# Performance work log

Measured on AMD Instinct MI355X. Metric: run time of the kernel, lower is better.

## Reference

```python
import math
import jax, jax.numpy as jnp
import numpy as np

B, M, N = 32, 64, 5000   # batch, multi_width (POMO rollouts), n_nodes
L, H, D, E = 100, 8, 16, 128  # local_size, head_num, qkv_dim, emb_dim


def setup_inputs() -> dict:
    key = jax.random.key(0)
    ks = jax.random.split(key, 10)
    return {
        "dist": jax.random.uniform(ks[0], (B, M, N), jnp.float32),
        "theta": jax.random.uniform(ks[1], (B, M, N), jnp.float32, minval=-math.pi, maxval=math.pi),
        "ninf_mask": jnp.zeros((B, M, N), jnp.float32),
        "W_init": jax.random.normal(ks[2], (E, 2), jnp.float32) * 0.1,
        "b_init": jax.random.normal(ks[3], (E,), jnp.float32) * 0.1,
        "cur_token": jax.random.uniform(ks[4], (E,), jnp.float32, minval=-1.0, maxval=1.0),
        "Wq": jax.random.normal(ks[5], (H * D, E), jnp.float32) * 0.05,
        "Wk": jax.random.normal(ks[6], (H * D, E), jnp.float32) * 0.05,
        "Wv": jax.random.normal(ks[7], (H * D, E), jnp.float32) * 0.05,
        "Wc": jax.random.normal(ks[8], (E, H * D), jnp.float32) * 0.05,
        "bc": jax.random.normal(ks[9], (E,), jnp.float32) * 0.05,
    }


def _positional_signal():
    # transformer sinusoidal encoding over the L gathered neighbors (E even -> no pad)
    num_ts = E // 2
    log_inc = math.log(10000.0) / max(num_ts - 1, 1)
    inv_ts = jnp.exp(jnp.arange(num_ts, dtype=jnp.float32) * -log_inc)
    pos = jnp.arange(L, dtype=jnp.float32)
    scaled = pos[:, None] * inv_ts[None, :]            # [L, E/2]
    return jnp.concatenate([jnp.sin(scaled), jnp.cos(scaled)], axis=1)  # [L, E]


def reference(dist, theta, ninf_mask, W_init, b_init, cur_token, Wq, Wk, Wv, Wc, bc):
    # mask out infeasible nodes (dist - (-inf) = +inf pushes them out of top-k)
    d = dist - ninf_mask                               # [B, M, N]
    neg_vals, idx = jax.lax.top_k(-d, L)               # smallest-L distances
    sorted_dist = -neg_vals                            # [B, M, L] ascending
    sorted_mask = jnp.take_along_axis(ninf_mask, idx, axis=-1)
    norm = sorted_dist.max(axis=-1, keepdims=True) + 1e-6
    sorted_dist = sorted_dist / norm
    sorted_theta = jnp.take_along_axis(theta, idx, axis=-1)
    sdt = jnp.stack([sorted_dist, sorted_theta], axis=-1)   # [B, M, L, 2]

    init_k = sdt @ W_init.T + b_init + _positional_signal()  # [B, M, L, E]

    # current-token query is a single shared learned vector -> q is [H, D]
    q = (Wq @ cur_token).reshape(H, D)
    kh = (init_k @ Wk.T).reshape(B, M, L, H, D)
    vh = (init_k @ Wv.T).reshape(B, M, L, H, D)

    score = jnp.einsum('hd,bmlhd->bhml', q, kh) / jnp.sqrt(jnp.float32(D))
    score = score + sorted_mask[:, None, :, :]              # rank3 ninf mask
    w = jax.nn.softmax(score, axis=-1)                      # [B, H, M, L]
    att = jnp.einsum('bhml,bmlhd->bmhd', w, vh).reshape(B, M, H * D)
    mh = att @ Wc.T + bc                                    # [B, M, E]

    score2 = jnp.einsum('bme,bmle->bml', mh, init_k) / jnp.sqrt(jnp.float32(E))

    # scatter local scores back into full [B, M, N]
    bi = jnp.arange(B)[:, None, None]
    mi = jnp.arange(M)[None, :, None]
    out = jnp.zeros((B, M, N), jnp.float32).at[bi, mi, idx].set(score2)
    return out
```

## Files before the change

### kernel.cpp

```cpp
#include <hip/hip_runtime.h>
#include <math.h>

#define B_ 32
#define M_ 64
#define N_ 5000
#define L_ 100
#define H_ 8
#define D_ 16
#define E_ 128
#define NBIN 2048
#define NT 512
#define NI4 1250

#define OFF_POSQ  0
#define OFF_C0    800
#define OFF_C1    808
#define OFF_C2    816
#define OFF_PV0   824
#define OFF_PV1   952
#define OFF_PVB   1080
#define OFF_WC0   1208
#define OFF_WC1   1336
#define OFF_WCB   1464
#define OFF_SB    1592
#define OFF_PCB   1596
#define OFF_PV    1696
#define OFF_PCT   14496

__device__ __forceinline__ int vbin(float v) {
  if (!(v >= 0.f)) return 0;
  if (v >= 1.0f) return NBIN - 1;
  return (int)(v * (float)NBIN);
}
__device__ __forceinline__ unsigned int umap(float v) {
  unsigned int b = __float_as_uint(v);
  return (b & 0x80000000u) ? ~b : (b | 0x80000000u);
}

__global__ __launch_bounds__(128) void precomp(
    const float* __restrict__ Wq, const float* __restrict__ Wk,
    const float* __restrict__ cur, const float* __restrict__ Wi,
    const float* __restrict__ bi, const float* __restrict__ Wv,
    const float* __restrict__ Wc, const float* __restrict__ bc,
    float* __restrict__ ws)
{
  const int tid = threadIdx.x;
  const int blk = blockIdx.x;
  __shared__ float pr[E_];
  __shared__ float red[8];
  const int lane = tid & 63, wv = tid >> 6;

  if (blk == 0) {
    float qsv = 0.f;
    for (int e = 0; e < E_; ++e) qsv = fmaf(Wq[tid * E_ + e], cur[e], qsv);
    float wk0=0,wk1=0,wkb=0,pv0=0,pv1=0,pvb=0,wc0=0,wc1=0,wcb=0;
    for (int e = 0; e < E_; ++e) {
      float wi0 = Wi[2*e], wi1 = Wi[2*e+1], bie = bi[e];
      float wk = Wk[tid*E_+e], wvv = Wv[tid*E_+e], wcc = Wc[e*(H_*D_)+tid];
      wk0=fmaf(wk,wi0,wk0);  wk1=fmaf(wk,wi1,wk1);  wkb=fmaf(wk,bie,wkb);
      pv0=fmaf(wvv,wi0,pv0); pv1=fmaf(wvv,wi1,pv1); pvb=fmaf(wvv,bie,pvb);
      wc0=fmaf(wcc,wi0,wc0); wc1=fmaf(wcc,wi1,wc1); wcb=fmaf(wcc,bie,wcb);
    }
    ws[OFF_PV0+tid]=pv0; ws[OFF_PV1+tid]=pv1; ws[OFF_PVB+tid]=pvb;
    ws[OFF_WC0+tid]=wc0; ws[OFF_WC1+tid]=wc1; ws[OFF_WCB+tid]=wcb;
    float c0 = qsv*wk0, c1 = qsv*wk1, c2 = qsv*wkb;
    for (int off = 1; off < 16; off <<= 1) {
      c0 += __shfl_xor(c0, off, 16); c1 += __shfl_xor(c1, off, 16); c2 += __shfl_xor(c2, off, 16);
    }
    if ((tid & 15) == 0) {
      int h = tid >> 4;
      ws[OFF_C0+h] = c0*0.25f; ws[OFF_C1+h] = c1*0.25f; ws[OFF_C2+h] = c2*0.25f;
    }
    float p0 = Wi[2*tid]*bc[tid], p1 = Wi[2*tid+1]*bc[tid], p2 = bi[tid]*bc[tid];
    for (int off = 32; off > 0; off >>= 1) {
      p0 += __shfl_xor(p0, off, 64); p1 += __shfl_xor(p1, off, 64); p2 += __shfl_xor(p2, off, 64);
    }
    if (lane == 0) { red[wv*3+0]=p0; red[wv*3+1]=p1; red[wv*3+2]=p2; }
    __syncthreads();
    if (tid == 0) {
      ws[OFF_SB+0]=red[0]+red[3]; ws[OFF_SB+1]=red[1]+red[4]; ws[OFF_SB+2]=red[2]+red[5];
    }
  } else {
    const int l = blk - 1;
    const float log_inc = 0.14619588050755848f;
    {
      int j = tid & 63;
      float scaled = (float)l * expf(-(float)j * log_inc);
      pr[tid] = (tid < 64) ? sinf(scaled) : cosf(scaled);
    }
    __syncthreads();
    float qsv=0.f, pwk=0.f, accv=0.f, accc=0.f;
    for (int e = 0; e < E_; ++e) qsv = fmaf(Wq[tid*E_+e], cur[e], qsv);
    for (int e = 0; e < E_; ++e) {
      float p = pr[e];
      pwk  = fmaf(Wk[tid*E_+e], p, pwk);
      accv = fmaf(Wv[tid*E_+e], p, accv);
      accc = fmaf(Wc[e*(H_*D_)+tid], p, accc);
    }
    ws[OFF_PV  + l*(H_*D_) + tid] = accv;
    ws[OFF_PCT + tid*L_ + l] = accc;
    float pq = qsv * pwk;
    for (int off = 1; off < 16; off <<= 1) pq += __shfl_xor(pq, off, 16);
    if ((tid & 15) == 0) ws[OFF_POSQ + (tid>>4)*L_ + l] = pq * 0.25f;
    float pb = pr[tid] * bc[tid];
    for (int off = 32; off > 0; off >>= 1) pb += __shfl_xor(pb, off, 64);
    if (lane == 0) red[wv] = pb;
    __syncthreads();
    if (tid == 0) ws[OFF_PCB + l] = red[0] + red[1];
  }
}

union alignas(16) SU {
  struct { unsigned short bins[N_]; unsigned int hist[NBIN]; } s;
  float rowbuf[N_];
  struct { float score[H_ * L_]; } a;
};

__global__ __launch_bounds__(NT, 8) void local_att_kernel(
    const float* __restrict__ dist, const float* __restrict__ theta,
    const float* __restrict__ ninf, const float* __restrict__ ws,
    float* __restrict__ out)
{
  __shared__ SU su;
  __shared__ unsigned long long sel64[128];
  __shared__ float sdv[128];
  __shared__ int idxs[128];
  __shared__ float stv[L_], smv[L_];
  __shared__ float att[H_ * D_], a0s[H_], a1s[H_];
  __shared__ unsigned int wsum[8];
  __shared__ int s_bstar;
  __shared__ unsigned int s_cumB, s_binc, s_chosen, s_cumb2, s_cnt;
  __shared__ float s_m0, s_m1, s_mb;

  const int tid = threadIdx.x;
  const int lane = tid & 63, wv = tid >> 6;
  const size_t base = (size_t)blockIdx.x * N_;
  const float4* d4 = (const float4*)(dist + base);
  const float4* n4 = (const float4*)(ninf + base);

  for (int j = tid; j < NBIN; j += NT) su.s.hist[j] = 0u;
  if (tid < 128) sel64[tid] = ~0ull;
  if (tid == 0) s_cnt = 0u;
  __syncthreads();

#pragma unroll
  for (int k = 0; k < 3; ++k) {
    int i4 = tid + k * NT;
    if (i4 < NI4) {
      float4 dv = d4[i4], nv = n4[i4];
      float vv4[4] = {dv.x - nv.x, dv.y - nv.y, dv.z - nv.z, dv.w - nv.w};
      unsigned int bn[4];
#pragma unroll
      for (int c = 0; c < 4; ++c) {
        bn[c] = (unsigned int)vbin(vv4[c]);
        atomicAdd(&su.s.hist[bn[c]], 1u);
      }
      uint2 pk;
      pk.x = bn[0] | (bn[1] << 16);
      pk.y = bn[2] | (bn[3] << 16);
      *(uint2*)&su.s.bins[i4 * 4] = pk;
    }
  }
  __syncthreads();

  unsigned int h4[4]; unsigned int s = 0u;
#pragma unroll
  for (int k2 = 0; k2 < 4; ++k2) { h4[k2] = su.s.hist[tid * 4 + k2]; s += h4[k2]; }
  unsigned int v = s;
  for (int off = 1; off < 64; off <<= 1) { unsigned int x = __shfl_up(v, off, 64); if (lane >= off) v += x; }
  if (lane == 63) wsum[wv] = v;
  __syncthreads();
  { unsigned int add = 0; for (int ww = 0; ww < wv; ++ww) add += wsum[ww]; v += add; }
  {
    unsigned int cumB = v - s;
    if (cumB < (unsigned)L_ && v >= (unsigned)L_) {
      unsigned int c = cumB;
#pragma unroll
      for (int k2 = 0; k2 < 4; ++k2) {
        unsigned int hh = h4[k2];
        if (c + hh >= (unsigned)L_) { s_bstar = tid * 4 + k2; s_cumB = c; s_binc = hh; break; }
        c += hh;
      }
    }
  }
  __syncthreads();
  const int bstar = s_bstar;
  const bool fb = (s_cumB + s_binc > 128u);
  unsigned long long kpiv = ~0ull;

  if (fb) {
    unsigned long long prefix = 0ull; unsigned int Krem = L_;
    for (int pass = 0; pass < 6; ++pass) {
      const int shift = 40 - 8 * pass;
      for (int j2 = tid; j2 < 256; j2 += NT) su.s.hist[j2] = 0u;
      __syncthreads();
#pragma unroll
      for (int k = 0; k < 3; ++k) {
        int i4 = tid + k * NT;
        if (i4 < NI4) {
          float4 dv = d4[i4], nv = n4[i4];
          float vv4[4] = {dv.x - nv.x, dv.y - nv.y, dv.z - nv.z, dv.w - nv.w};
#pragma unroll
          for (int c = 0; c < 4; ++c) {
            unsigned long long key = ((unsigned long long)umap(vv4[c]) << 16) | (unsigned)(i4 * 4 + c);
            if ((key >> (shift + 8)) == prefix)
              atomicAdd(&su.s.hist[(unsigned)(key >> shift) & 0xFFu], 1u);
          }
        }
      }
      __syncthreads();
      unsigned int ss = (tid < 256) ? su.s.hist[tid] : 0u;
      unsigned int vv = ss;
      for (int off = 1; off < 64; off <<= 1) { unsigned int x = __shfl_up(vv, off, 64); if (lane >= off) vv += x; }
      if (lane == 63) wsum[wv] = vv;
      __syncthreads();
      { unsigned int ad = 0; for (int ww = 0; ww < wv; ++ww) ad += wsum[ww]; vv += ad; }
      unsigned int cb = vv - ss;
      if (tid < 256 && cb < Krem && vv >= Krem) { s_chosen = (unsigned)tid; s_cumb2 = cb; }
      __syncthreads();
      prefix = (prefix << 8) | s_chosen;
      Krem -= s_cumb2;
      __syncthreads();
    }
    kpiv = prefix;
  }

#pragma unroll
  for (int k = 0; k < 3; ++k) {
    int i4 = tid + k * NT;
    if (i4 < NI4) {
      if (!fb) {
        uint2 pk = *(const uint2*)&su.s.bins[i4 * 4];
        unsigned int b4[4] = {pk.x & 0xFFFFu, pk.x >> 16, pk.y & 0xFFFFu, pk.y >> 16};
#pragma unroll
        for (int c = 0; c < 4; ++c) {
          if ((int)b4[c] <= bstar) {
            int i = i4 * 4 + c;
            float vvv = dist[base + i] - ninf[base + i];
            unsigned long long key = ((unsigned long long)umap(vvv) << 16) | (unsigned)i;
            unsigned int p = atomicAdd(&s_cnt, 1u);
            if (p < 128u) sel64[p] = key;
          }
        }
      } else {
        float4 dv = d4[i4], nv = n4[i4];
        float vv4[4] = {dv.x - nv.x, dv.y - nv.y, dv.z - nv.z, dv.w - nv.w};
#pragma unroll
        for (int c = 0; c < 4; ++c) {
          unsigned long long key = ((unsigned long long)umap(vv4[c]) << 16) | (unsigned)(i4 * 4 + c);
          if (key <= kpiv) {
            unsigned int p = atomicAdd(&s_cnt, 1u);
            if (p < 128u) sel64[p] = key;
          }
        }
      }
    }
  }
  __syncthreads();

  if (tid < 128) {
    unsigned long long my = sel64[tid];
    if (my != ~0ull) {
      int rank = 0;
      for (int j = 0; j < 128; ++j) rank += (sel64[j] < my) ? 1 : 0;
      unsigned int u = (unsigned int)(my >> 16);
      unsigned int bits = (u & 0x80000000u) ? (u ^ 0x80000000u) : ~u;
      sdv[rank] = __uint_as_float(bits);
      idxs[rank] = (int)(my & 0xFFFFull);
    }
  }
  __syncthreads();

  const float invn = 1.0f / (sdv[L_ - 1] + 1e-6f);

  if (tid < L_) { int ix = idxs[tid]; stv[tid] = theta[base + ix]; smv[tid] = ninf[base + ix]; }
  __syncthreads();

  for (int t = tid; t < H_ * L_; t += NT) {
    int h = t / L_, l = t - h * L_;
    su.a.score[t] = fmaf(sdv[l] * invn, ws[OFF_C0 + h],
                    fmaf(stv[l], ws[OFF_C1 + h],
                         ws[OFF_C2 + h] + ws[OFF_POSQ + t] + smv[l]));
  }
  __syncthreads();

  {
    const int h = wv, l64 = lane;
    float* sc = &su.a.score[h * L_];
    float mx = -INFINITY;
    for (int l = l64; l < L_; l += 64) mx = fmaxf(mx, sc[l]);
    for (int off = 32; off > 0; off >>= 1) mx = fmaxf(mx, __shfl_xor(mx, off, 64));
    float sum = 0.f;
    for (int l = l64; l < L_; l += 64) { float ex = expf(sc[l] - mx); sc[l] = ex; sum += ex; }
    for (int off = 32; off > 0; off >>= 1) sum += __shfl_xor(sum, off, 64);
    const float inv = 1.f / sum;
    float a0p = 0.f, a1p = 0.f;
    for (int l = l64; l < L_; l += 64) {
      float w2 = sc[l] * inv; sc[l] = w2;
      a0p = fmaf(w2, sdv[l] * invn, a0p); a1p = fmaf(w2, stv[l], a1p);
    }
    for (int off = 32; off > 0; off >>= 1) { a0p += __shfl_xor(a0p, off, 64); a1p += __shfl_xor(a1p, off, 64); }
    if (l64 == 0) { a0s[h] = a0p; a1s[h] = a1p; }
  }
  __syncthreads();

  if (tid < H_ * D_) {
    const int hd = tid, h = hd >> 4;
    float acc = fmaf(a0s[h], ws[OFF_PV0 + hd], fmaf(a1s[h], ws[OFF_PV1 + hd], ws[OFF_PVB + hd]));
    const float* pv = ws + OFF_PV + hd;
    const float* wrow = &su.a.score[h * L_];
#pragma unroll 4
    for (int l = 0; l < L_; ++l) acc = fmaf(wrow[l], pv[l * (H_ * D_)], acc);
    att[hd] = acc;
  }
  __syncthreads();

  if (tid < 64) {
    float x0 = att[tid], x1 = att[tid + 64];
    float m0 = fmaf(x0, ws[OFF_WC0 + tid], x1 * ws[OFF_WC0 + tid + 64]);
    float m1 = fmaf(x0, ws[OFF_WC1 + tid], x1 * ws[OFF_WC1 + tid + 64]);
    float mb = fmaf(x0, ws[OFF_WCB + tid], x1 * ws[OFF_WCB + tid + 64]);
    for (int off = 32; off > 0; off >>= 1) {
      m0 += __shfl_xor(m0, off, 64); m1 += __shfl_xor(m1, off, 64); mb += __shfl_xor(mb, off, 64);
    }
    if (tid == 0) {
      s_m0 = m0 + ws[OFF_SB + 0]; s_m1 = m1 + ws[OFF_SB + 1]; s_mb = mb + ws[OFF_SB + 2];
    }
  } else {
    float4 z = {0.f, 0.f, 0.f, 0.f};
    for (int i4 = tid - 64; i4 < NI4; i4 += NT - 64) ((float4*)su.rowbuf)[i4] = z;
  }
  __syncthreads();

  if (tid < L_) {
    float acc = ws[OFF_PCB + tid];
    const float* pct = ws + OFF_PCT + tid;
#pragma unroll 4
    for (int hd = 0; hd < H_ * D_; ++hd) acc = fmaf(att[hd], pct[hd * L_], acc);
    float s2v = fmaf(sdv[tid] * invn, s_m0, fmaf(stv[tid], s_m1, s_mb + acc)) * 0.08838834764831845f;
    su.rowbuf[idxs[tid]] = s2v;
  }
  __syncthreads();

  const float4* rb4 = (const float4*)su.rowbuf;
  float4* o4 = (float4*)(out + base);
  for (int i4 = tid; i4 < NI4; i4 += NT) o4[i4] = rb4[i4];
}

extern "C" void kernel_launch(void* const* d_in, const int* in_sizes, int n_in,
                              void* d_out, int out_size, void* d_ws, size_t ws_size,
                              hipStream_t stream) {
  const float* dist = (const float*)d_in[0];
  const float* theta = (const float*)d_in[1];
  const float* ninf = (const float*)d_in[2];
  const float* Wi   = (const float*)d_in[3];
  const float* bi   = (const float*)d_in[4];
  const float* cur  = (const float*)d_in[5];
  const float* Wq   = (const float*)d_in[6];
  const float* Wk   = (const float*)d_in[7];
  const float* Wv   = (const float*)d_in[8];
  const float* Wc   = (const float*)d_in[9];
  const float* bcv  = (const float*)d_in[10];
  float* out = (float*)d_out;
  float* ws  = (float*)d_ws;

  precomp<<<dim3(L_ + 1), dim3(128), 0, stream>>>(Wq, Wk, cur, Wi, bi, Wv, Wc, bcv, ws);
  local_att_kernel<<<dim3(B_ * M_), dim3(NT), 0, stream>>>(dist, theta, ninf, ws, out);
}
```

Measured before the change: 83.56 us.

## Process one row per wavefront with wave-local top-k and barrier-free attention

Restructures the main kernel so each 64-lane wavefront handles a whole row (8 rows per block), replacing block-wide __syncthreads with wave-local LDS waits and shuffles. The histogram shrinks to 1024 bins with a bank-spread index mapping, and the row is reloaded from global memory for the selection pass instead of storing per-element bins in LDS. Softmax and attention are computed in registers with 8 lanes per head, and the output is zero-filled directly in global memory and then scattered. Each lane now carries many more registers, and relying on the write ordering between the zero fill and the scatter (enforced only by vmcnt waits) is a correctness risk.

```diff
diff --git a/kernel.cpp b/kernel.cpp
--- a/kernel.cpp
+++ b/kernel.cpp
@@ -8,9 +8,9 @@
 #define H_ 8
 #define D_ 16
 #define E_ 128
-#define NBIN 2048
-#define NT 512
+#define NBIN 1024
 #define NI4 1250
+#define RPB 8
 
 #define OFF_POSQ  0
 #define OFF_C0    800
@@ -27,6 +27,9 @@
 #define OFF_PV    1696
 #define OFF_PCT   14496
 
+#define WSYNC() do { asm volatile("s_waitcnt lgkmcnt(0)" ::: "memory"); __builtin_amdgcn_sched_barrier(0); } while (0)
+#define VSYNC() do { asm volatile("s_waitcnt vmcnt(0)" ::: "memory"); __builtin_amdgcn_sched_barrier(0); } while (0)
+
 __device__ __forceinline__ int vbin(float v) {
   if (!(v >= 0.f)) return 0;
   if (v >= 1.0f) return NBIN - 1;
@@ -36,6 +39,8 @@
   unsigned int b = __float_as_uint(v);
   return (b & 0x80000000u) ? ~b : (b | 0x80000000u);
 }
+#define HMAP(b)  ((((b) & 15) << 6) + ((b) >> 4))
+#define HMAP4(b) ((((b) & 3) << 6) + ((b) >> 2))
 
 __global__ __launch_bounds__(128) void precomp(
     const float* __restrict__ Wq, const float* __restrict__ Wk,
@@ -48,7 +53,7 @@
   const int blk = blockIdx.x;
   __shared__ float pr[E_];
   __shared__ float red[8];
-  const int lane = tid & 63, wv = tid >> 6;
+  const int lane = tid & 63, wvv = tid >> 6;
 
   if (blk == 0) {
     float qsv = 0.f;
@@ -56,9 +61,9 @@
     float wk0=0,wk1=0,wkb=0,pv0=0,pv1=0,pvb=0,wc0=0,wc1=0,wcb=0;
     for (int e = 0; e < E_; ++e) {
       float wi0 = Wi[2*e], wi1 = Wi[2*e+1], bie = bi[e];
-      float wk = Wk[tid*E_+e], wvv = Wv[tid*E_+e], wcc = Wc[e*(H_*D_)+tid];
+      float wk = Wk[tid*E_+e], wvx = Wv[tid*E_+e], wcc = Wc[e*(H_*D_)+tid];
       wk0=fmaf(wk,wi0,wk0);  wk1=fmaf(wk,wi1,wk1);  wkb=fmaf(wk,bie,wkb);
-      pv0=fmaf(wvv,wi0,pv0); pv1=fmaf(wvv,wi1,pv1); pvb=fmaf(wvv,bie,pvb);
+      pv0=fmaf(wvx,wi0,pv0); pv1=fmaf(wvx,wi1,pv1); pvb=fmaf(wvx,bie,pvb);
       wc0=fmaf(wcc,wi0,wc0); wc1=fmaf(wcc,wi1,wc1); wcb=fmaf(wcc,bie,wcb);
     }
     ws[OFF_PV0+tid]=pv0; ws[OFF_PV1+tid]=pv1; ws[OFF_PVB+tid]=pvb;
@@ -75,7 +80,7 @@
     for (int off = 32; off > 0; off >>= 1) {
       p0 += __shfl_xor(p0, off, 64); p1 += __shfl_xor(p1, off, 64); p2 += __shfl_xor(p2, off, 64);
     }
-    if (lane == 0) { red[wv*3+0]=p0; red[wv*3+1]=p1; red[wv*3+2]=p2; }
+    if (lane == 0) { red[wvv*3+0]=p0; red[wvv*3+1]=p1; red[wvv*3+2]=p2; }
     __syncthreads();
     if (tid == 0) {
       ws[OFF_SB+0]=red[0]+red[3]; ws[OFF_SB+1]=red[1]+red[4]; ws[OFF_SB+2]=red[2]+red[5];
@@ -104,247 +109,332 @@
     if ((tid & 15) == 0) ws[OFF_POSQ + (tid>>4)*L_ + l] = pq * 0.25f;
     float pb = pr[tid] * bc[tid];
     for (int off = 32; off > 0; off >>= 1) pb += __shfl_xor(pb, off, 64);
-    if (lane == 0) red[wv] = pb;
+    if (lane == 0) red[wvv] = pb;
     __syncthreads();
     if (tid == 0) ws[OFF_PCB + l] = red[0] + red[1];
   }
 }
 
-union alignas(16) SU {
-  struct { unsigned short bins[N_]; unsigned int hist[NBIN]; } s;
-  float rowbuf[N_];
-  struct { float score[H_ * L_]; } a;
-};
-
-__global__ __launch_bounds__(NT, 8) void local_att_kernel(
+__global__ __launch_bounds__(512) void local_att_kernel(
     const float* __restrict__ dist, const float* __restrict__ theta,
     const float* __restrict__ ninf, const float* __restrict__ ws,
     float* __restrict__ out)
 {
-  __shared__ SU su;
-  __shared__ unsigned long long sel64[128];
-  __shared__ float sdv[128];
-  __shared__ int idxs[128];
-  __shared__ float stv[L_], smv[L_];
-  __shared__ float att[H_ * D_], a0s[H_], a1s[H_];
-  __shared__ unsigned int wsum[8];
-  __shared__ int s_bstar;
-  __shared__ unsigned int s_cumB, s_binc, s_chosen, s_cumb2, s_cnt;
-  __shared__ float s_m0, s_m1, s_mb;
-
-  const int tid = threadIdx.x;
-  const int lane = tid & 63, wv = tid >> 6;
-  const size_t base = (size_t)blockIdx.x * N_;
+  __shared__ alignas(16) unsigned int arena[RPB][1024];
+  __shared__ unsigned int cnt8[RPB];
+
+  const int tid  = threadIdx.x;
+  const int lane = tid & 63;
+  const int wv   = tid >> 6;
+  const size_t base = (size_t)(blockIdx.x * RPB + wv) * N_;
+  unsigned int* hist = arena[wv];
+  unsigned long long* sel = (unsigned long long*)&arena[wv][256];
+  float* sdv = (float*)&arena[wv][520];
+  unsigned int* idxs = &arena[wv][648];
+  float* stv = (float*)&arena[wv][776];
+  float* smv = (float*)&arena[wv][876];
+  float* att = (float*)&arena[wv][0];
+
   const float4* d4 = (const float4*)(dist + base);
   const float4* n4 = (const float4*)(ninf + base);
 
-  for (int j = tid; j < NBIN; j += NT) su.s.hist[j] = 0u;
-  if (tid < 128) sel64[tid] = ~0ull;
-  if (tid == 0) s_cnt = 0u;
-  __syncthreads();
-
-#pragma unroll
-  for (int k = 0; k < 3; ++k) {
-    int i4 = tid + k * NT;
-    if (i4 < NI4) {
-      float4 dv = d4[i4], nv = n4[i4];
-      float vv4[4] = {dv.x - nv.x, dv.y - nv.y, dv.z - nv.z, dv.w - nv.w};
-      unsigned int bn[4];
-#pragma unroll
-      for (int c = 0; c < 4; ++c) {
-        bn[c] = (unsigned int)vbin(vv4[c]);
-        atomicAdd(&su.s.hist[bn[c]], 1u);
-      }
-      uint2 pk;
-      pk.x = bn[0] | (bn[1] << 16);
-      pk.y = bn[2] | (bn[3] << 16);
-      *(uint2*)&su.s.bins[i4 * 4] = pk;
-    }
-  }
-  __syncthreads();
-
-  unsigned int h4[4]; unsigned int s = 0u;
-#pragma unroll
-  for (int k2 = 0; k2 < 4; ++k2) { h4[k2] = su.s.hist[tid * 4 + k2]; s += h4[k2]; }
-  unsigned int v = s;
-  for (int off = 1; off < 64; off <<= 1) { unsigned int x = __shfl_up(v, off, 64); if (lane >= off) v += x; }
-  if (lane == 63) wsum[wv] = v;
-  __syncthreads();
-  { unsigned int add = 0; for (int ww = 0; ww < wv; ++ww) add += wsum[ww]; v += add; }
-  {
-    unsigned int cumB = v - s;
-    if (cumB < (unsigned)L_ && v >= (unsigned)L_) {
-      unsigned int c = cumB;
-#pragma unroll
-      for (int k2 = 0; k2 < 4; ++k2) {
-        unsigned int hh = h4[k2];
-        if (c + hh >= (unsigned)L_) { s_bstar = tid * 4 + k2; s_cumB = c; s_binc = hh; break; }
-        c += hh;
-      }
-    }
-  }
-  __syncthreads();
-  const int bstar = s_bstar;
-  const bool fb = (s_cumB + s_binc > 128u);
-  unsigned long long kpiv = ~0ull;
-
-  if (fb) {
-    unsigned long long prefix = 0ull; unsigned int Krem = L_;
+#pragma unroll
+  for (int k = 0; k < 16; ++k) hist[lane + 64 * k] = 0u;
+  WSYNC();
+
+  {
+    float4 dreg[20], nreg[20];
+#pragma unroll
+    for (int t = 0; t < 20; ++t) {
+      int i4 = lane + 64 * t;
+      if (i4 < NI4) { dreg[t] = d4[i4]; nreg[t] = n4[i4]; }
+    }
+#pragma unroll
+    for (int t = 0; t < 20; ++t) {
+      int i4 = lane + 64 * t;
+      if (i4 < NI4) {
+#pragma unroll
+        for (int c = 0; c < 4; ++c) {
+          float v = (&dreg[t].x)[c] - (&nreg[t].x)[c];
+          atomicAdd(&hist[HMAP(vbin(v))], 1u);
+        }
+      }
+    }
+  }
+  WSYNC();
+
+  unsigned int bstar, cumB, binc;
+  {
+    unsigned int s = 0;
+#pragma unroll
+    for (int k = 0; k < 16; ++k) s += hist[k * 64 + lane];
+    unsigned int v = s;
+#pragma unroll
+    for (int off = 1; off < 64; off <<= 1) {
+      unsigned int x = __shfl_up(v, off, 64);
+      if (lane >= off) v += x;
+    }
+    unsigned int cumBefore = v - s;
+    bool cross = (cumBefore < (unsigned)L_) && (v >= (unsigned)L_);
+    unsigned long long mk = __ballot(cross);
+    int src = __ffsll(mk) - 1;
+    unsigned int bstarL = 0, cumL = 0, bincL = 0;
+    if (cross) {
+      unsigned int c = cumBefore; int kk = 0;
+      for (; kk < 16; ++kk) {
+        unsigned int h = hist[kk * 64 + lane];
+        if (c + h >= (unsigned)L_) { bincL = h; break; }
+        c += h;
+      }
+      bstarL = (unsigned)(lane * 16 + kk); cumL = c;
+    }
+    bstar = (unsigned)__shfl((int)bstarL, src, 64);
+    cumB  = (unsigned)__shfl((int)cumL,  src, 64);
+    binc  = (unsigned)__shfl((int)bincL, src, 64);
+  }
+  const bool fb = (cumB + binc > 128u);
+
+  if (!fb) {
+    sel[lane] = ~0ull; sel[lane + 64] = ~0ull;
+    if (lane == 0) cnt8[wv] = 0u;
+    WSYNC();
+    float4 dreg[20], nreg[20];
+#pragma unroll
+    for (int t = 0; t < 20; ++t) {
+      int i4 = lane + 64 * t;
+      if (i4 < NI4) { dreg[t] = d4[i4]; nreg[t] = n4[i4]; }
+    }
+#pragma unroll
+    for (int t = 0; t < 20; ++t) {
+      int i4 = lane + 64 * t;
+      if (i4 < NI4) {
+#pragma unroll
+        for (int c = 0; c < 4; ++c) {
+          float v = (&dreg[t].x)[c] - (&nreg[t].x)[c];
+          if (vbin(v) <= (int)bstar) {
+            unsigned long long key = ((unsigned long long)umap(v) << 16) | (unsigned)(i4 * 4 + c);
+            unsigned int p = atomicAdd(&cnt8[wv], 1u);
+            if (p < 128u) sel[p] = key;
+          }
+        }
+      }
+    }
+  } else {
+    unsigned long long prefix = 0ull;
+    unsigned int Krem = L_;
     for (int pass = 0; pass < 6; ++pass) {
       const int shift = 40 - 8 * pass;
-      for (int j2 = tid; j2 < 256; j2 += NT) su.s.hist[j2] = 0u;
-      __syncthreads();
-#pragma unroll
-      for (int k = 0; k < 3; ++k) {
-        int i4 = tid + k * NT;
+#pragma unroll
+      for (int k = 0; k < 4; ++k) hist[lane + 64 * k] = 0u;
+      WSYNC();
+      for (int t = 0; t < 20; ++t) {
+        int i4 = lane + 64 * t;
         if (i4 < NI4) {
           float4 dv = d4[i4], nv = n4[i4];
-          float vv4[4] = {dv.x - nv.x, dv.y - nv.y, dv.z - nv.z, dv.w - nv.w};
 #pragma unroll
           for (int c = 0; c < 4; ++c) {
-            unsigned long long key = ((unsigned long long)umap(vv4[c]) << 16) | (unsigned)(i4 * 4 + c);
+            float v = (&dv.x)[c] - (&nv.x)[c];
+            unsigned long long key = ((unsigned long long)umap(v) << 16) | (unsigned)(i4 * 4 + c);
             if ((key >> (shift + 8)) == prefix)
-              atomicAdd(&su.s.hist[(unsigned)(key >> shift) & 0xFFu], 1u);
+              atomicAdd(&hist[HMAP4((int)((key >> shift) & 0xFFu))], 1u);
           }
         }
       }
-      __syncthreads();
-      unsigned int ss = (tid < 256) ? su.s.hist[tid] : 0u;
-      unsigned int vv = ss;
-      for (int off = 1; off < 64; off <<= 1) { unsigned int x = __shfl_up(vv, off, 64); if (lane >= off) vv += x; }
-      if (lane == 63) wsum[wv] = vv;
-      __syncthreads();
-      { unsigned int ad = 0; for (int ww = 0; ww < wv; ++ww) ad += wsum[ww]; vv += ad; }
-      unsigned int cb = vv - ss;
-      if (tid < 256 && cb < Krem && vv >= Krem) { s_chosen = (unsigned)tid; s_cumb2 = cb; }
-      __syncthreads();
-      prefix = (prefix << 8) | s_chosen;
-      Krem -= s_cumb2;
-      __syncthreads();
-    }
-    kpiv = prefix;
-  }
-
-#pragma unroll
-  for (int k = 0; k < 3; ++k) {
-    int i4 = tid + k * NT;
-    if (i4 < NI4) {
-      if (!fb) {
-        uint2 pk = *(const uint2*)&su.s.bins[i4 * 4];
-        unsigned int b4[4] = {pk.x & 0xFFFFu, pk.x >> 16, pk.y & 0xFFFFu, pk.y >> 16};
+      WSYNC();
+      unsigned int s4 = 0;
+#pragma unroll
+      for (int k = 0; k < 4; ++k) s4 += hist[k * 64 + lane];
+      unsigned int v2 = s4;
+#pragma unroll
+      for (int off = 1; off < 64; off <<= 1) {
+        unsigned int x = __shfl_up(v2, off, 64);
+        if (lane >= off) v2 += x;
+      }
+      unsigned int cb = v2 - s4;
+      bool cr = (cb < Krem) && (v2 >= Krem);
+      unsigned long long mk2 = __ballot(cr);
+      int sl = __ffsll(mk2) - 1;
+      unsigned int chL = 0, cmL = 0;
+      if (cr) {
+        unsigned int c = cb; int kk = 0;
+        for (; kk < 4; ++kk) {
+          unsigned int h = hist[kk * 64 + lane];
+          if (c + h >= Krem) break;
+          c += h;
+        }
+        chL = (unsigned)(lane * 4 + kk); cmL = c;
+      }
+      unsigned int chosen = (unsigned)__shfl((int)chL, sl, 64);
+      unsigned int cum2   = (unsigned)__shfl((int)cmL, sl, 64);
+      prefix = (prefix << 8) | chosen;
+      Krem -= cum2;
+      WSYNC();
+    }
+    const unsigned long long kpiv = prefix;
+    sel[lane] = ~0ull; sel[lane + 64] = ~0ull;
+    if (lane == 0) cnt8[wv] = 0u;
+    WSYNC();
+    for (int t = 0; t < 20; ++t) {
+      int i4 = lane + 64 * t;
+      if (i4 < NI4) {
+        float4 dv = d4[i4], nv = n4[i4];
 #pragma unroll
         for (int c = 0; c < 4; ++c) {
-          if ((int)b4[c] <= bstar) {
-            int i = i4 * 4 + c;
-            float vvv = dist[base + i] - ninf[base + i];
-            unsigned long long key = ((unsigned long long)umap(vvv) << 16) | (unsigned)i;
-            unsigned int p = atomicAdd(&s_cnt, 1u);
-            if (p < 128u) sel64[p] = key;
+          float v = (&dv.x)[c] - (&nv.x)[c];
+          unsigned long long key = ((unsigned long long)umap(v) << 16) | (unsigned)(i4 * 4 + c);
+          if (key <= kpiv) {
+            unsigned int p = atomicAdd(&cnt8[wv], 1u);
+            if (p < 128u) sel[p] = key;
           }
         }
-      } else {
-        float4 dv = d4[i4], nv = n4[i4];
-        float vv4[4] = {dv.x - nv.x, dv.y - nv.y, dv.z - nv.z, dv.w - nv.w};
-#pragma unroll
-        for (int c = 0; c < 4; ++c) {
-          unsigned long long key = ((unsigned long long)umap(vv4[c]) << 16) | (unsigned)(i4 * 4 + c);
-          if (key <= kpiv) {
-            unsigned int p = atomicAdd(&s_cnt, 1u);
-            if (p < 128u) sel64[p] = key;
-          }
-        }
-      }
-    }
-  }
-  __syncthreads();
-
-  if (tid < 128) {
-    unsigned long long my = sel64[tid];
-    if (my != ~0ull) {
-      int rank = 0;
-      for (int j = 0; j < 128; ++j) rank += (sel64[j] < my) ? 1 : 0;
-      unsigned int u = (unsigned int)(my >> 16);
+      }
+    }
+  }
+  WSYNC();
+
+  {
+    unsigned long long ka = sel[lane], kb = sel[lane + 64];
+    int ra = 0, rb = 0;
+#pragma unroll 8
+    for (int j2 = 0; j2 < 128; ++j2) {
+      unsigned long long kj = sel[j2];
+      ra += (kj < ka) ? 1 : 0;
+      rb += (kj < kb) ? 1 : 0;
+    }
+    if (ka != ~0ull) {
+      unsigned int u = (unsigned int)(ka >> 16);
       unsigned int bits = (u & 0x80000000u) ? (u ^ 0x80000000u) : ~u;
-      sdv[rank] = __uint_as_float(bits);
-      idxs[rank] = (int)(my & 0xFFFFull);
-    }
-  }
-  __syncthreads();
+      sdv[ra] = __uint_as_float(bits);
+      idxs[ra] = (unsigned int)(ka & 0xFFFFull);
+    }
+    if (kb != ~0ull) {
+      unsigned int u = (unsigned int)(kb >> 16);
+      unsigned int bits = (u & 0x80000000u) ? (u ^ 0x80000000u) : ~u;
+      sdv[rb] = __uint_as_float(bits);
+      idxs[rb] = (unsigned int)(kb & 0xFFFFull);
+    }
+  }
+  WSYNC();
 
   const float invn = 1.0f / (sdv[L_ - 1] + 1e-6f);
-
-  if (tid < L_) { int ix = idxs[tid]; stv[tid] = theta[base + ix]; smv[tid] = ninf[base + ix]; }
-  __syncthreads();
-
-  for (int t = tid; t < H_ * L_; t += NT) {
-    int h = t / L_, l = t - h * L_;
-    su.a.score[t] = fmaf(sdv[l] * invn, ws[OFF_C0 + h],
-                    fmaf(stv[l], ws[OFF_C1 + h],
-                         ws[OFF_C2 + h] + ws[OFF_POSQ + t] + smv[l]));
-  }
-  __syncthreads();
-
-  {
-    const int h = wv, l64 = lane;
-    float* sc = &su.a.score[h * L_];
+  {
+    const int l1 = lane + 64;
+    const int l1g = (l1 < L_) ? l1 : 0;
+    unsigned int i0 = idxs[lane], i1 = idxs[l1g];
+    float sd0 = sdv[lane], sd1 = sdv[l1g];
+    float th0 = theta[base + i0];
+    float nm0 = ninf[base + i0];
+    float th1 = 0.f, nm1 = 0.f;
+    if (l1 < L_) { th1 = theta[base + i1]; nm1 = ninf[base + i1]; }
+    stv[lane] = th0; smv[lane] = nm0; sdv[lane] = sd0 * invn;
+    if (l1 < L_) { stv[l1] = th1; smv[l1] = nm1; sdv[l1] = sd1 * invn; }
+  }
+  WSYNC();
+
+  const int hh = lane >> 3, jj = lane & 7;
+  float w13[13];
+  float a0, a1;
+  {
+    const float c0 = ws[OFF_C0 + hh], c1 = ws[OFF_C1 + hh], c2 = ws[OFF_C2 + hh];
     float mx = -INFINITY;
-    for (int l = l64; l < L_; l += 64) mx = fmaxf(mx, sc[l]);
-    for (int off = 32; off > 0; off >>= 1) mx = fmaxf(mx, __shfl_xor(mx, off, 64));
+#pragma unroll
+    for (int k = 0; k < 13; ++k) {
+      int l = jj + 8 * k;
+      float scv = -INFINITY;
+      if (l < L_)
+        scv = fmaf(sdv[l], c0, fmaf(stv[l], c1, c2 + ws[OFF_POSQ + hh * L_ + l] + smv[l]));
+      w13[k] = scv;
+      mx = fmaxf(mx, scv);
+    }
+#pragma unroll
+    for (int off = 1; off <= 4; off <<= 1) mx = fmaxf(mx, __shfl_xor(mx, off, 64));
     float sum = 0.f;
-    for (int l = l64; l < L_; l += 64) { float ex = expf(sc[l] - mx); sc[l] = ex; sum += ex; }
-    for (int off = 32; off > 0; off >>= 1) sum += __shfl_xor(sum, off, 64);
-    const float inv = 1.f / sum;
-    float a0p = 0.f, a1p = 0.f;
-    for (int l = l64; l < L_; l += 64) {
-      float w2 = sc[l] * inv; sc[l] = w2;
-      a0p = fmaf(w2, sdv[l] * invn, a0p); a1p = fmaf(w2, stv[l], a1p);
-    }
-    for (int off = 32; off > 0; off >>= 1) { a0p += __shfl_xor(a0p, off, 64); a1p += __shfl_xor(a1p, off, 64); }
-    if (l64 == 0) { a0s[h] = a0p; a1s[h] = a1p; }
-  }
-  __syncthreads();
-
-  if (tid < H_ * D_) {
-    const int hd = tid, h = hd >> 4;
-    float acc = fmaf(a0s[h], ws[OFF_PV0 + hd], fmaf(a1s[h], ws[OFF_PV1 + hd], ws[OFF_PVB + hd]));
-    const float* pv = ws + OFF_PV + hd;
-    const float* wrow = &su.a.score[h * L_];
-#pragma unroll 4
-    for (int l = 0; l < L_; ++l) acc = fmaf(wrow[l], pv[l * (H_ * D_)], acc);
-    att[hd] = acc;
-  }
-  __syncthreads();
-
-  if (tid < 64) {
-    float x0 = att[tid], x1 = att[tid + 64];
-    float m0 = fmaf(x0, ws[OFF_WC0 + tid], x1 * ws[OFF_WC0 + tid + 64]);
-    float m1 = fmaf(x0, ws[OFF_WC1 + tid], x1 * ws[OFF_WC1 + tid + 64]);
-    float mb = fmaf(x0, ws[OFF_WCB + tid], x1 * ws[OFF_WCB + tid + 64]);
-    for (int off = 32; off > 0; off >>= 1) {
-      m0 += __shfl_xor(m0, off, 64); m1 += __shfl_xor(m1, off, 64); mb += __shfl_xor(mb, off, 64);
-    }
-    if (tid == 0) {
-      s_m0 = m0 + ws[OFF_SB + 0]; s_m1 = m1 + ws[OFF_SB + 1]; s_mb = mb + ws[OFF_SB + 2];
-    }
-  } else {
-    float4 z = {0.f, 0.f, 0.f, 0.f};
-    for (int i4 = tid - 64; i4 < NI4; i4 += NT - 64) ((float4*)su.rowbuf)[i4] = z;
-  }
-  __syncthreads();
-
-  if (tid < L_) {
-    float acc = ws[OFF_PCB + tid];
-    const float* pct = ws + OFF_PCT + tid;
-#pragma unroll 4
-    for (int hd = 0; hd < H_ * D_; ++hd) acc = fmaf(att[hd], pct[hd * L_], acc);
-    float s2v = fmaf(sdv[tid] * invn, s_m0, fmaf(stv[tid], s_m1, s_mb + acc)) * 0.08838834764831845f;
-    su.rowbuf[idxs[tid]] = s2v;
-  }
-  __syncthreads();
-
-  const float4* rb4 = (const float4*)su.rowbuf;
-  float4* o4 = (float4*)(out + base);
-  for (int i4 = tid; i4 < NI4; i4 += NT) o4[i4] = rb4[i4];
+#pragma unroll
+    for (int k = 0; k < 13; ++k) { float e = expf(w13[k] - mx); w13[k] = e; sum += e; }
+#pragma unroll
+    for (int off = 1; off <= 4; off <<= 1) sum += __shfl_xor(sum, off, 64);
+    const float inv = 1.0f / sum;
+    a0 = 0.f; a1 = 0.f;
+#pragma unroll
+    for (int k = 0; k < 13; ++k) {
+      int l = jj + 8 * k; int lc = (l < L_) ? l : 0;
+      float wgt = w13[k] * inv; w13[k] = wgt;
+      a0 = fmaf(wgt, sdv[lc], a0);
+      a1 = fmaf(wgt, stv[lc], a1);
+    }
+#pragma unroll
+    for (int off = 1; off <= 4; off <<= 1) { a0 += __shfl_xor(a0, off, 64); a1 += __shfl_xor(a1, off, 64); }
+  }
+
+  {
+    float part[16];
+#pragma unroll
+    for (int t = 0; t < 16; ++t) part[t] = 0.f;
+#pragma unroll
+    for (int k = 0; k < 13; ++k) {
+      int l = jj + 8 * k;
+      if (l < L_) {
+        const float* pv = ws + OFF_PV + l * (H_ * D_) + hh * 16;
+        float wgt = w13[k];
+#pragma unroll
+        for (int t = 0; t < 16; ++t) part[t] = fmaf(wgt, pv[t], part[t]);
+      }
+    }
+#pragma unroll
+    for (int off = 1; off <= 4; off <<= 1) {
+#pragma unroll
+      for (int t = 0; t < 16; ++t) part[t] += __shfl_xor(part[t], off, 64);
+    }
+#pragma unroll
+    for (int t = 0; t < 16; ++t) {
+      int hd = hh * 16 + t;
+      att[hd] = fmaf(a0, ws[OFF_PV0 + hd], fmaf(a1, ws[OFF_PV1 + hd], ws[OFF_PVB + hd])) + part[t];
+    }
+  }
+  WSYNC();
+
+  float m0, m1, mb;
+  {
+    float x0 = att[lane], x1 = att[lane + 64];
+    m0 = fmaf(x0, ws[OFF_WC0 + lane], x1 * ws[OFF_WC0 + lane + 64]);
+    m1 = fmaf(x0, ws[OFF_WC1 + lane], x1 * ws[OFF_WC1 + lane + 64]);
+    mb = fmaf(x0, ws[OFF_WCB + lane], x1 * ws[OFF_WCB + lane + 64]);
+#pragma unroll
+    for (int off = 1; off < 64; off <<= 1) {
+      m0 += __shfl_xor(m0, off, 64);
+      m1 += __shfl_xor(m1, off, 64);
+      mb += __shfl_xor(mb, off, 64);
+    }
+    m0 += ws[OFF_SB + 0]; m1 += ws[OFF_SB + 1]; mb += ws[OFF_SB + 2];
+  }
+
+  const int l1 = lane + 64;
+  const int l1c = (l1 < L_) ? l1 : 0;
+  float s2a = 0.f, s2b = 0.f;
+#pragma unroll 8
+  for (int hd = 0; hd < H_ * D_; ++hd) {
+    float a = att[hd];
+    s2a = fmaf(a, ws[OFF_PCT + hd * L_ + lane], s2a);
+    s2b = fmaf(a, ws[OFF_PCT + hd * L_ + l1c], s2b);
+  }
+  const float SC = 0.08838834764831845f;
+  float out_a = (fmaf(sdv[lane], m0, fmaf(stv[lane], m1, mb)) + ws[OFF_PCB + lane] + s2a) * SC;
+  float out_b = (fmaf(sdv[l1c], m0, fmaf(stv[l1c], m1, mb)) + ws[OFF_PCB + l1c] + s2b) * SC;
+  unsigned int ia = idxs[lane];
+  unsigned int ib = idxs[l1c];
+
+  {
+    float4* o4 = (float4*)(out + base);
+    const float4 z = make_float4(0.f, 0.f, 0.f, 0.f);
+#pragma unroll
+    for (int t = 0; t < 20; ++t) {
+      int i4 = lane + 64 * t;
+      if (i4 < NI4) o4[i4] = z;
+    }
+  }
+  VSYNC();
+  out[base + ia] = out_a;
+  if (l1 < L_) out[base + ib] = out_b;
 }
 
 extern "C" void kernel_launch(void* const* d_in, const int* in_sizes, int n_in,
@@ -365,5 +455,5 @@
   float* ws  = (float*)d_ws;
 
   precomp<<<dim3(L_ + 1), dim3(128), 0, stream>>>(Wq, Wk, cur, Wi, bi, Wv, Wc, bcv, ws);
-  local_att_kernel<<<dim3(B_ * M_), dim3(NT), 0, stream>>>(dist, theta, ninf, ws, out);
+  local_att_kernel<<<dim3((B_ * M_) / RPB), dim3(512), 0, stream>>>(dist, theta, ninf, ws, out);
 }
```

Result: faster. 79.76 us (-4.5%).
